# Performance work log

Measured on AMD Instinct MI355X. Metric: run time of the kernel, lower is better.

## Reference

```python
import jax, jax.numpy as jnp
import numpy as np
from jax import lax

B, C, H, W = 16, 3, 64, 64
P = 256        # total_patches
PS = 9         # patch_size
E = 256        # attn_embed_dim
NH = 8         # attn_heads
POSD = 64      # pos_embed_dim
HW = H * W
DH = E // NH


def setup_inputs() -> dict:
    key = jax.random.key(0)
    ks = jax.random.split(key, 20)
    def rn(k, shape, fan_in):
        return jax.random.normal(k, shape, jnp.float32) * (1.0 / np.sqrt(fan_in))
    return {
        "x": jax.random.normal(ks[0], (B, C, H, W), jnp.float32),
        "conv_w": rn(ks[1], (P, C, PS, PS), C * PS * PS),
        "conv_b": jnp.zeros((P,), jnp.float32),
        "in_w": rn(ks[2], (HW, E), HW),
        "in_b": jnp.zeros((E,), jnp.float32),
        "wq": rn(ks[3], (E, E), E), "bq": jnp.zeros((E,), jnp.float32),
        "wk": rn(ks[4], (E, E), E), "bk": jnp.zeros((E,), jnp.float32),
        "wv": rn(ks[5], (E, E), E), "bv": jnp.zeros((E,), jnp.float32),
        "wo": rn(ks[6], (E, E), E), "bo": jnp.zeros((E,), jnp.float32),
        "out_w": rn(ks[7], (E, HW), E),
        "out_b": jnp.zeros((HW,), jnp.float32),
        "fc_w": rn(ks[8], (HW, 2), HW),
        "fc_b": jnp.zeros((2,), jnp.float32),
        "pos_w": rn(ks[9], (2, POSD), 2),
        "pos_b": jnp.zeros((POSD,), jnp.float32),
    }


# pixel-center normalized coords matching affine_grid(align_corners=False)
_BASE = (2.0 * jnp.arange(PS, dtype=jnp.float32) + 1.0) / PS - 1.0


def _sample_patch(img, tx, ty):
    # img: (C,H,W); tx, ty scalars. Replicates affine_grid + grid_sample
    # (bilinear, padding_mode='border', align_corners=False) WITHOUT the
    # full-image repeat of the original module.
    gx = (PS / W) * _BASE[None, :] + tx     # (PS,PS) x-coords
    gy = (PS / H) * _BASE[:, None] + ty     # (PS,PS) y-coords
    ix = ((gx + 1.0) * W - 1.0) * 0.5       # unnormalize, align_corners=False
    iy = ((gy + 1.0) * H - 1.0) * 0.5
    x0 = jnp.floor(ix); y0 = jnp.floor(iy)
    wx = ix - x0;       wy = iy - y0
    x0i = jnp.clip(x0.astype(jnp.int32), 0, W - 1)
    x1i = jnp.clip(x0.astype(jnp.int32) + 1, 0, W - 1)
    y0i = jnp.clip(y0.astype(jnp.int32), 0, H - 1)
    y1i = jnp.clip(y0.astype(jnp.int32) + 1, 0, H - 1)
    v00 = img[:, y0i, x0i]; v01 = img[:, y0i, x1i]
    v10 = img[:, y1i, x0i]; v11 = img[:, y1i, x1i]
    return (v00 * (1 - wx) * (1 - wy) + v01 * wx * (1 - wy)
            + v10 * (1 - wx) * wy + v11 * wx * wy)   # (C,PS,PS)


def _forward(x, conv_w, conv_b, in_w, in_b, wq, bq, wk, bk, wv, bv, wo, bo,
             out_w, out_b, fc_w, fc_b, pos_w, pos_b):
    # ConvBlock: conv (same padding for odd kernel) + ReLU
    feat = lax.conv_general_dilated(
        x, conv_w, (1, 1), [(PS // 2, PS // 2)] * 2,
        dimension_numbers=("NCHW", "OIHW", "NCHW"))
    feat = jax.nn.relu(feat + conv_b[None, :, None, None])   # (B,P,H,W)
    # ConvSelfAttn: tokens are the P channels, features are flattened HxW
    tok = feat.reshape(B, P, HW) @ in_w + in_b                # (B,P,E)
    q = (tok @ wq + bq).reshape(B, P, NH, DH)
    k = (tok @ wk + bk).reshape(B, P, NH, DH)
    v = (tok @ wv + bv).reshape(B, P, NH, DH)
    scores = jnp.einsum("bqhd,bkhd->bhqk", q, k) / np.sqrt(DH)
    attn = jax.nn.softmax(scores, axis=-1)
    o = jnp.einsum("bhqk,bkhd->bqhd", attn, v).reshape(B, P, E)
    o = o @ wo + bo
    feat2 = o @ out_w + out_b                                 # (B,P,HW)
    # translation params in [-1,1]
    tp = jnp.tanh(feat2 @ fc_w + fc_b)                        # (B,P,2)
    tx, ty = tp[..., 0], tp[..., 1]
    sample_bp = jax.vmap(jax.vmap(_sample_patch, in_axes=(None, 0, 0)),
                         in_axes=(0, 0, 0))
    patches = sample_bp(x, tx, ty)                            # (B,P,C,PS,PS)
    patches = patches.reshape(B, P, C * PS * PS)
    pos_embeds = tp @ pos_w + pos_b                           # (B,P,POSD)
    return patches, pos_embeds


def reference(x, conv_w, conv_b, in_w, in_b, wq, bq, wk, bk, wv, bv, wo, bo,
              out_w, out_b, fc_w, fc_b, pos_w, pos_b):
    return _forward(x, conv_w, conv_b, in_w, in_b, wq, bq, wk, bk, wv, bv,
                    wo, bo, out_w, out_b, fc_w, fc_b, pos_w, pos_b)
```

## Files before the change

kernel.cpp:

```cpp
#include <hip/hip_runtime.h>
#include <hip/hip_bf16.h>

#define Bd 16
#define Cd 3
#define Hd 64
#define Wd 64
#define Pd 256
#define PSd 9
#define Ed 256
#define NHd 8
#define DHd 32
#define HWd 4096
#define POSDd 64

typedef unsigned short u16;
typedef short short8 __attribute__((ext_vector_type(8)));
typedef float f32x4 __attribute__((ext_vector_type(4)));

__device__ __forceinline__ float bf2f(u16 u) {
    union { unsigned int i; float f; } c; c.i = ((unsigned int)u) << 16; return c.f;
}
__device__ __forceinline__ u16 f2bf(float f) {
    unsigned int x = __float_as_uint(f);
    unsigned int r = (x + 0x7fffu + ((x >> 16) & 1u)) >> 16;
    return (u16)r;
}

__global__ __launch_bounds__(256) void prep_fused(
    const float* __restrict__ conv_w, const float* __restrict__ in_w,
    const float* __restrict__ wq, const float* __restrict__ wk,
    const float* __restrict__ wv, const float* __restrict__ bq,
    const float* __restrict__ bk, const float* __restrict__ bv,
    const float* __restrict__ out_w, const float* __restrict__ fc_w,
    const float* __restrict__ out_b, const float* __restrict__ fc_b,
    u16* __restrict__ convw_h, u16* __restrict__ convw_l,
    u16* __restrict__ inw_h, u16* __restrict__ inw_l,
    u16* __restrict__ wqkv_h, u16* __restrict__ wqkv_l,
    float* __restrict__ bqkv, float* __restrict__ G, float* __restrict__ h0) {
    __shared__ u16 th[64][65];
    __shared__ u16 tl[64][65];
    int blk = blockIdx.x, t = threadIdx.x;

    if (blk < 256) {
        float v = (t < 243) ? conv_w[blk * 243 + t] : 0.f;
        u16 h = f2bf(v);
        convw_h[blk * 256 + t] = h;
        convw_l[blk * 256 + t] = f2bf(v - bf2f(h));
    } else if (blk < 560) {
        const float* W;
        u16 *Th, *Tl;
        int K, local;
        if (blk < 272)      { W = wq;   Th = wqkv_h;              Tl = wqkv_l;              K = 256;  local = blk - 256; }
        else if (blk < 288) { W = wk;   Th = wqkv_h + 256 * 256;  Tl = wqkv_l + 256 * 256;  K = 256;  local = blk - 272; }
        else if (blk < 304) { W = wv;   Th = wqkv_h + 512 * 256;  Tl = wqkv_l + 512 * 256;  K = 256;  local = blk - 288; }
        else                { W = in_w; Th = inw_h;               Tl = inw_l;               K = 4096; local = blk - 304; }
        int kt = (K == 256) ? (local & 3) : (local & 63);
        int nt = (K == 256) ? (local >> 2) : (local >> 6);
        int k0 = kt * 64, n0 = nt * 64;
        int col = t & 63, r4 = t >> 6;
        #pragma unroll
        for (int i = 0; i < 16; i++) {
            int kr = 4 * i + r4;
            float v = W[(size_t)(k0 + kr) * 256 + n0 + col];
            u16 h = f2bf(v);
            th[col][kr] = h;
            tl[col][kr] = f2bf(v - bf2f(h));
        }
        __syncthreads();
        #pragma unroll
        for (int i = 0; i < 16; i++) {
            int nr = 4 * i + r4;
            Th[(size_t)(n0 + nr) * K + k0 + col] = th[nr][col];
            Tl[(size_t)(n0 + nr) * K + k0 + col] = tl[nr][col];
        }
    } else if (blk == 560) {
        bqkv[t] = bq[t]; bqkv[256 + t] = bk[t]; bqkv[512 + t] = bv[t];
    } else if (blk < 625) {
        int e = (blk - 561) * 4 + (t >> 6);
        int lane = t & 63;
        float a0 = 0.f, a1 = 0.f;
        for (int i = lane; i < HWd; i += 64) {
            float a = out_w[(size_t)e * HWd + i];
            a0 += a * fc_w[2 * i];
            a1 += a * fc_w[2 * i + 1];
        }
        #pragma unroll
        for (int off = 32; off; off >>= 1) { a0 += __shfl_xor(a0, off); a1 += __shfl_xor(a1, off); }
        if (lane == 0) { G[2 * e] = a0; G[2 * e + 1] = a1; }
    } else {
        int wj = t >> 6, lane = t & 63;
        if (wj < 2) {
            float a = 0.f;
            for (int i = lane; i < HWd; i += 64) a += out_b[i] * fc_w[2 * i + wj];
            #pragma unroll
            for (int off = 32; off; off >>= 1) a += __shfl_xor(a, off);
            if (lane == 0) h0[wj] = a + fc_b[wj];
        }
    }
}

__global__ __launch_bounds__(64) void precompute_M2(
    const float* __restrict__ wo, const float* __restrict__ bo,
    const float* __restrict__ G, float* __restrict__ M2, float* __restrict__ h0) {
    int blk = blockIdx.x, lane = threadIdx.x;
    if (blk < 256) {
        float m0 = 0.f, m1 = 0.f;
        for (int f = lane; f < Ed; f += 64) {
            float wv = wo[blk * Ed + f];
            m0 += wv * G[2 * f];
            m1 += wv * G[2 * f + 1];
        }
        #pragma unroll
        for (int off = 32; off; off >>= 1) { m0 += __shfl_xor(m0, off); m1 += __shfl_xor(m1, off); }
        if (lane == 0) { M2[2 * blk] = m0; M2[2 * blk + 1] = m1; }
    } else {
        int j = blk - 256;
        float hh = 0.f;
        for (int f = lane; f < Ed; f += 64) hh += bo[f] * G[2 * f + j];
        #pragma unroll
        for (int off = 32; off; off >>= 1) hh += __shfl_xor(hh, off);
        if (lane == 0) h0[j] += hh;
    }
}

__global__ __launch_bounds__(256, 3) void conv_gemm(
    const u16* __restrict__ Ah, const u16* __restrict__ Al,
    const float* __restrict__ x, const float* __restrict__ conv_b,
    u16* __restrict__ feat_hi, u16* __restrict__ feat_lo) {
    __shared__ u16 sBh[64 * 72], sBl[64 * 72];
    __shared__ float wls[3 * 9 * 72];
    int tid = threadIdx.x;
    int w = tid >> 6, L = tid & 63;
    int m16 = L & 15, qd = L >> 4;
    int y = blockIdx.x;
    int nb = y << 6;
    int b = blockIdx.y;

    for (int i = tid; i < 3 * 9 * 72; i += 256) wls[i] = 0.f;
    __syncthreads();
    for (int i = tid; i < 3 * 9 * 64; i += 256) {
        int c = i / 576, rem = i - c * 576, wr = rem >> 6, col = rem & 63;
        int iy = y - 4 + wr;
        if (iy >= 0 && iy < 64)
            wls[c * 648 + wr * 72 + 4 + col] = x[((b * 3 + c) << 12) + (iy << 6) + col];
    }
    __syncthreads();

    f32x4 acc[4][4];
    #pragma unroll
    for (int mt = 0; mt < 4; mt++)
        #pragma unroll
        for (int ct = 0; ct < 4; ct++) acc[mt][ct] = (f32x4){0.f, 0.f, 0.f, 0.f};

    int n = tid >> 2, kb = (tid & 3) << 4;
    int arow = w * 16 + m16;

    u16 hbuf[16] __attribute__((aligned(8)));
    u16 lbuf[16] __attribute__((aligned(8)));
    auto build = [&](int kbase) {
        #pragma unroll
        for (int j = 0; j < 16; j++) {
            int k = kbase + kb + j;
            float v = 0.f;
            if (k < 243) {
                int c = (k >= 81) + (k >= 162);
                int rem = k - c * 81;
                int dy = (rem * 57) >> 9;
                int dx = rem - dy * 9;
                v = wls[c * 648 + dy * 72 + dx + n];
            }
            u16 h = f2bf(v);
            hbuf[j] = h;
            lbuf[j] = f2bf(v - bf2f(h));
        }
    };
    build(0);

    for (int k0 = 0; k0 < 256; k0 += 64) {
        short8 afh[4][2], afl[4][2];
        #pragma unroll
        for (int mt = 0; mt < 4; mt++)
            #pragma unroll
            for (int c = 0; c < 2; c++) {
                int ao = (mt * 64 + arow) * 256 + k0 + c * 32 + qd * 8;
                afh[mt][c] = *(const short8*)(Ah + ao);
                afl[mt][c] = *(const short8*)(Al + ao);
            }
        __syncthreads();
        #pragma unroll
        for (int t = 0; t < 4; t++) {
            *(ushort4*)&sBh[n * 72 + kb + 4 * t] = *(ushort4*)&hbuf[4 * t];
            *(ushort4*)&sBl[n * 72 + kb + 4 * t] = *(ushort4*)&lbuf[4 * t];
        }
        __syncthreads();
        if (k0 < 192) build(k0 + 64);
        #pragma unroll
        for (int c = 0; c < 2; c++) {
            #pragma unroll
            for (int ct = 0; ct < 4; ct++) {
                int bb = (ct * 16 + m16) * 72 + c * 32 + qd * 8;
                short8 bH = *(const short8*)&sBh[bb];
                short8 bL = *(const short8*)&sBl[bb];
                #pragma unroll
                for (int mt = 0; mt < 4; mt++) {
                    acc[mt][ct] = __builtin_amdgcn_mfma_f32_16x16x32_bf16(afh[mt][c], bH, acc[mt][ct], 0, 0, 0);
                    acc[mt][ct] = __builtin_amdgcn_mfma_f32_16x16x32_bf16(afh[mt][c], bL, acc[mt][ct], 0, 0, 0);
                    acc[mt][ct] = __builtin_amdgcn_mfma_f32_16x16x32_bf16(afl[mt][c], bH, acc[mt][ct], 0, 0, 0);
                }
            }
        }
    }

    #pragma unroll
    for (int mt = 0; mt < 4; mt++) {
        #pragma unroll
        for (int i = 0; i < 4; i++) {
            int gr = mt * 64 + w * 16 + qd * 4 + i;
            float bv = conv_b[gr];
            #pragma unroll
            for (int ct = 0; ct < 4; ct++) {
                int gc = nb + ct * 16 + m16;
                float val = fmaxf(acc[mt][ct][i] + bv, 0.f);
                size_t oi = ((size_t)(b * 256 + gr)) * HWd + gc;
                u16 h = f2bf(val);
                feat_hi[oi] = h;
                feat_lo[oi] = f2bf(val - bf2f(h));
            }
        }
    }
}

__global__ __launch_bounds__(256, 4) void gemm_mfma3(
    const u16* __restrict__ Ah, const u16* __restrict__ Al,
    const u16* __restrict__ Bh, const u16* __restrict__ Bl,
    const float* __restrict__ bias,
    float* __restrict__ Co, u16* __restrict__ Ch, u16* __restrict__ Cl,
    int N, int K, int klen, long long pstride, int mode) {
    __shared__ u16 sAh[64 * 72], sAl[64 * 72], sBh[64 * 72], sBl[64 * 72];
    int tid = threadIdx.x;
    int w = tid >> 6;
    int L = tid & 63;
    int m16 = L & 15, qd = L >> 4;
    int mb = blockIdx.y * 64, nb = blockIdx.x * 64;
    int kbeg = blockIdx.z * klen;

    f32x4 acc[4];
    #pragma unroll
    for (int i = 0; i < 4; i++) acc[i] = (f32x4){0.f, 0.f, 0.f, 0.f};

    int r = tid >> 2, s = tid & 3;
    const u16* pAh = Ah + (size_t)(mb + r) * K + kbeg + s * 16;
    const u16* pAl = Al + (size_t)(mb + r) * K + kbeg + s * 16;
    const u16* pBh = Bh + (size_t)(nb + r) * K + kbeg + s * 16;
    const u16* pBl = Bl + (size_t)(nb + r) * K + kbeg + s * 16;
    u16* dAh = &sAh[r * 72 + s * 16];
    u16* dAl = &sAl[r * 72 + s * 16];
    u16* dBh = &sBh[r * 72 + s * 16];
    u16* dBl = &sBl[r * 72 + s * 16];

    uint4 a0 = *(const uint4*)(pAh);
    uint4 a1 = *(const uint4*)(pAh + 8);
    uint4 a2 = *(const uint4*)(pAl);
    uint4 a3 = *(const uint4*)(pAl + 8);
    uint4 b0 = *(const uint4*)(pBh);
    uint4 b1 = *(const uint4*)(pBh + 8);
    uint4 b2 = *(const uint4*)(pBl);
    uint4 b3 = *(const uint4*)(pBl + 8);

    for (int k0 = 0; k0 < klen; k0 += 64) {
        __syncthreads();
        *(uint4*)(dAh) = a0; *(uint4*)(dAh + 8) = a1;
        *(uint4*)(dAl) = a2; *(uint4*)(dAl + 8) = a3;
        *(uint4*)(dBh) = b0; *(uint4*)(dBh + 8) = b1;
        *(uint4*)(dBl) = b2; *(uint4*)(dBl + 8) = b3;
        __syncthreads();
        int kn = k0 + 64;
        if (kn < klen) {
            a0 = *(const uint4*)(pAh + kn);
            a1 = *(const uint4*)(pAh + kn + 8);
            a2 = *(const uint4*)(pAl + kn);
            a3 = *(const uint4*)(pAl + kn + 8);
            b0 = *(const uint4*)(pBh + kn);
            b1 = *(const uint4*)(pBh + kn + 8);
            b2 = *(const uint4*)(pBl + kn);
            b3 = *(const uint4*)(pBl + kn + 8);
        }
        #pragma unroll
        for (int c = 0; c < 2; c++) {
            int ab = (w * 16 + m16) * 72 + c * 32 + qd * 8;
            short8 aH = *(const short8*)&sAh[ab];
            short8 aL = *(const short8*)&sAl[ab];
            #pragma unroll
            for (int ct = 0; ct < 4; ct++) {
                int bb = (ct * 16 + m16) * 72 + c * 32 + qd * 8;
                short8 bH = *(const short8*)&sBh[bb];
                short8 bL = *(const short8*)&sBl[bb];
                acc[ct] = __builtin_amdgcn_mfma_f32_16x16x32_bf16(aH, bH, acc[ct], 0, 0, 0);
                acc[ct] = __builtin_amdgcn_mfma_f32_16x16x32_bf16(aH, bL, acc[ct], 0, 0, 0);
                acc[ct] = __builtin_amdgcn_mfma_f32_16x16x32_bf16(aL, bH, acc[ct], 0, 0, 0);
            }
        }
    }

    #pragma unroll
    for (int ct = 0; ct < 4; ct++) {
        int gc = nb + ct * 16 + m16;
        float bv = (mode == 2) ? 0.f : bias[gc];
        #pragma unroll
        for (int i = 0; i < 4; i++) {
            int gr = mb + w * 16 + qd * 4 + i;
            float val = acc[ct][i] + bv;
            size_t oi = (size_t)gr * N + gc;
            if (mode == 0) {
                Co[oi] = val;
            } else if (mode == 2) {
                Co[(size_t)blockIdx.z * pstride + oi] = val;
            } else {
                u16 h = f2bf(val);
                Ch[oi] = h;
                Cl[oi] = f2bf(val - bf2f(h));
            }
        }
    }
}

__global__ __launch_bounds__(256) void reduce_split(
    const float* __restrict__ part, const float* __restrict__ bias,
    u16* __restrict__ Ch, u16* __restrict__ Cl, int total) {
    int i = (blockIdx.x * 256 + threadIdx.x) * 4;
    if (i >= total) return;
    float4 s0 = *(const float4*)(part + i);
    float4 s1 = *(const float4*)(part + (size_t)total + i);
    float4 s2 = *(const float4*)(part + 2 * (size_t)total + i);
    float4 s3 = *(const float4*)(part + 3 * (size_t)total + i);
    float4 bv = *(const float4*)(bias + (i & 255));
    float v[4] = { s0.x + s1.x + s2.x + s3.x + bv.x,
                   s0.y + s1.y + s2.y + s3.y + bv.y,
                   s0.z + s1.z + s2.z + s3.z + bv.z,
                   s0.w + s1.w + s2.w + s3.w + bv.w };
    u16 hb[4] __attribute__((aligned(8)));
    u16 lb[4] __attribute__((aligned(8)));
    #pragma unroll
    for (int j = 0; j < 4; j++) {
        u16 h = f2bf(v[j]);
        hb[j] = h;
        lb[j] = f2bf(v[j] - bf2f(h));
    }
    *(ushort4*)(Ch + i) = *(ushort4*)hb;
    *(ushort4*)(Cl + i) = *(ushort4*)lb;
}

__global__ __launch_bounds__(256) void transpose_v(
    const u16* __restrict__ qkvh, const u16* __restrict__ qkvl,
    u16* __restrict__ vTh, u16* __restrict__ vTl) {
    __shared__ u16 th[32][264];
    __shared__ u16 tl[32][264];
    int b = blockIdx.x, h = blockIdx.y;
    int t = threadIdx.x;
    {
        const u16* srch = qkvh + ((size_t)(b * 256 + t)) * 768 + 512 + h * 32;
        const u16* srcl = qkvl + ((size_t)(b * 256 + t)) * 768 + 512 + h * 32;
        #pragma unroll
        for (int j = 0; j < 4; j++) {
            short8 vh = *(const short8*)(srch + j * 8);
            short8 vl = *(const short8*)(srcl + j * 8);
            #pragma unroll
            for (int e = 0; e < 8; e++) {
                th[j * 8 + e][t] = (u16)vh[e];
                tl[j * 8 + e][t] = (u16)vl[e];
            }
        }
    }
    __syncthreads();
    {
        int d = t >> 3, seg = t & 7;
        size_t dst = ((size_t)((b * 8 + h) * 32 + d)) * 256 + seg * 32;
        #pragma unroll
        for (int j = 0; j < 4; j++) {
            *(uint4*)(vTh + dst + j * 8) = *(uint4*)&th[d][seg * 32 + j * 8];
            *(uint4*)(vTl + dst + j * 8) = *(uint4*)&tl[d][seg * 32 + j * 8];
        }
    }
}

__global__ __launch_bounds__(256) void attention_mfma(
    const u16* __restrict__ qkvh, const u16* __restrict__ qkvl,
    const u16* __restrict__ vTh, const u16* __restrict__ vTl,
    float* __restrict__ o) {
    __shared__ u16 ph[4][16][264];
    int b = blockIdx.x, h = blockIdx.y, qc = blockIdx.z;
    int tid = threadIdx.x;
    int w = tid >> 6, L = tid & 63;
    int m16 = L & 15, qd = L >> 4;
    const float rs = 0.17677669529663687f;

    size_t qoff = ((size_t)(b * 256 + qc * 64 + w * 16 + m16)) * 768 + h * 32 + qd * 8;
    short8 qH = *(const short8*)(qkvh + qoff);
    short8 qL = *(const short8*)(qkvl + qoff);

    f32x4 sacc[16];
    #pragma unroll
    for (int nt = 0; nt < 16; nt++) {
        size_t koff = ((size_t)(b * 256 + nt * 16 + m16)) * 768 + 256 + h * 32 + qd * 8;
        short8 bH = *(const short8*)(qkvh + koff);
        short8 bL = *(const short8*)(qkvl + koff);
        f32x4 a = (f32x4){0.f, 0.f, 0.f, 0.f};
        a = __builtin_amdgcn_mfma_f32_16x16x32_bf16(qH, bH, a, 0, 0, 0);
        a = __builtin_amdgcn_mfma_f32_16x16x32_bf16(qH, bL, a, 0, 0, 0);
        a = __builtin_amdgcn_mfma_f32_16x16x32_bf16(qL, bH, a, 0, 0, 0);
        sacc[nt] = a;
    }

    float l4[4] = {0.f, 0.f, 0.f, 0.f};
    #pragma unroll
    for (int nt = 0; nt < 16; nt++)
        #pragma unroll
        for (int i = 0; i < 4; i++) {
            float p = __expf(sacc[nt][i] * rs);
            sacc[nt][i] = p;
            l4[i] += p;
        }
    #pragma unroll
    for (int i = 0; i < 4; i++) {
        l4[i] += __shfl_xor(l4[i], 1);
        l4[i] += __shfl_xor(l4[i], 2);
        l4[i] += __shfl_xor(l4[i], 4);
        l4[i] += __shfl_xor(l4[i], 8);
    }

    #pragma unroll
    for (int nt = 0; nt < 16; nt++)
        #pragma unroll
        for (int i = 0; i < 4; i++)
            ph[w][qd * 4 + i][nt * 16 + m16] = f2bf(sacc[nt][i]);

    f32x4 oacc[2];
    oacc[0] = (f32x4){0.f, 0.f, 0.f, 0.f};
    oacc[1] = (f32x4){0.f, 0.f, 0.f, 0.f};
    size_t vbase = ((size_t)(b * 8 + h)) * 32 * 256;
    #pragma unroll
    for (int kt = 0; kt < 8; kt++) {
        short8 pa = *(const short8*)&ph[w][m16][kt * 32 + qd * 8];
        #pragma unroll
        for (int ct = 0; ct < 2; ct++) {
            size_t voff = vbase + (size_t)(ct * 16 + m16) * 256 + kt * 32 + qd * 8;
            short8 vH = *(const short8*)(vTh + voff);
            short8 vL = *(const short8*)(vTl + voff);
            oacc[ct] = __builtin_amdgcn_mfma_f32_16x16x32_bf16(pa, vH, oacc[ct], 0, 0, 0);
            oacc[ct] = __builtin_amdgcn_mfma_f32_16x16x32_bf16(pa, vL, oacc[ct], 0, 0, 0);
        }
    }

    #pragma unroll
    for (int i = 0; i < 4; i++) {
        float rinv = 1.f / l4[i];
        int orow = b * 256 + qc * 64 + w * 16 + qd * 4 + i;
        #pragma unroll
        for (int ct = 0; ct < 2; ct++)
            o[(size_t)orow * 256 + h * 32 + ct * 16 + m16] = oacc[ct][i] * rinv;
    }
}

#define PATCH_OUT 995328
__global__ __launch_bounds__(256) void head_kernel(
    const float* __restrict__ o, const float* __restrict__ M2,
    const float* __restrict__ h0, const float* __restrict__ pos_w,
    const float* __restrict__ pos_b, const float* __restrict__ x,
    float* __restrict__ out) {
    int w = threadIdx.x >> 6, lane = threadIdx.x & 63;
    int bp = blockIdx.x * 4 + w;
    int b = bp >> 8;

    const float* orow = o + (size_t)bp * Ed;
    float4 o4 = *(const float4*)(orow + lane * 4);
    int e0 = lane * 4;
    float s0 = o4.x * M2[2 * e0 + 0] + o4.y * M2[2 * e0 + 2] + o4.z * M2[2 * e0 + 4] + o4.w * M2[2 * e0 + 6];
    float s1 = o4.x * M2[2 * e0 + 1] + o4.y * M2[2 * e0 + 3] + o4.z * M2[2 * e0 + 5] + o4.w * M2[2 * e0 + 7];
    #pragma unroll
    for (int off = 32; off; off >>= 1) { s0 += __shfl_xor(s0, off); s1 += __shfl_xor(s1, off); }

    float tx = tanhf(s0 + h0[0]);
    float ty = tanhf(s1 + h0[1]);

    {
        float pv = tx * pos_w[lane] + ty * pos_w[64 + lane] + pos_b[lane];
        out[PATCH_OUT + bp * POSDd + lane] = pv;
    }

    const float* xb = x + b * 3 * HWd;
    #pragma unroll
    for (int s = 0; s < 4; s++) {
        int idx = s * 64 + lane;
        if (idx < 243) {
            int c = idx / 81;
            int rem = idx - c * 81;
            int iy = rem / 9;
            int jx = rem - iy * 9;
            float basex = (2.f * jx + 1.f) / 9.f - 1.f;
            float basey = (2.f * iy + 1.f) / 9.f - 1.f;
            float gx = 0.140625f * basex + tx;
            float gy = 0.140625f * basey + ty;
            float ix  = ((gx + 1.f) * 64.f - 1.f) * 0.5f;
            float iyf = ((gy + 1.f) * 64.f - 1.f) * 0.5f;
            float x0f = floorf(ix), y0f = floorf(iyf);
            float wx = ix - x0f, wy = iyf - y0f;
            int x0i = min(max((int)x0f, 0), 63);
            int x1i = min(max((int)x0f + 1, 0), 63);
            int y0i = min(max((int)y0f, 0), 63);
            int y1i = min(max((int)y0f + 1, 0), 63);
            const float* xc = xb + c * HWd;
            float v00 = xc[y0i * Wd + x0i];
            float v01 = xc[y0i * Wd + x1i];
            float v10 = xc[y1i * Wd + x0i];
            float v11 = xc[y1i * Wd + x1i];
            float val = v00 * (1.f - wx) * (1.f - wy) + v01 * wx * (1.f - wy)
                      + v10 * (1.f - wx) * wy + v11 * wx * wy;
            out[bp * 243 + idx] = val;
        }
    }
}

extern "C" void kernel_launch(void* const* d_in, const int* in_sizes, int n_in,
                              void* d_out, int out_size, void* d_ws, size_t ws_size,
                              hipStream_t stream) {
    (void)in_sizes; (void)n_in; (void)out_size;
    const float* x      = (const float*)d_in[0];
    const float* conv_w = (const float*)d_in[1];
    const float* conv_b = (const float*)d_in[2];
    const float* in_w   = (const float*)d_in[3];
    const float* in_b   = (const float*)d_in[4];
    const float* wq     = (const float*)d_in[5];
    const float* bq     = (const float*)d_in[6];
    const float* wk     = (const float*)d_in[7];
    const float* bk     = (const float*)d_in[8];
    const float* wv     = (const float*)d_in[9];
    const float* bv     = (const float*)d_in[10];
    const float* wo     = (const float*)d_in[11];
    const float* bo     = (const float*)d_in[12];
    const float* out_w  = (const float*)d_in[13];
    const float* out_b  = (const float*)d_in[14];
    const float* fc_w   = (const float*)d_in[15];
    const float* fc_b   = (const float*)d_in[16];
    const float* pos_w  = (const float*)d_in[17];
    const float* pos_b  = (const float*)d_in[18];

    int CB = 16;
    for (;;) {
        size_t u16e = (size_t)(2 * CB + 4) * 1048576 + 2 * 196608 + 2 * 65536
                    + 2 * 3145728 + 2 * 1048576;
        size_t f32e = 768 + 1048576 + 4ull * CB * 65536 + 2048;
        if (u16e * 2 + f32e * 4 <= ws_size || CB == 1) break;
        CB >>= 1;
    }
    int nchunks = 16 / CB;

    char* base = (char*)d_ws;
    u16* feat_hi = (u16*)base;
    u16* feat_lo = feat_hi + (size_t)CB * 1048576;
    u16* tok_hi  = feat_lo + (size_t)CB * 1048576;
    u16* tok_lo  = tok_hi + 1048576;
    u16* inw_h   = tok_lo + 1048576;
    u16* inw_l   = inw_h + 1048576;
    u16* wqkv_h  = inw_l + 1048576;
    u16* wqkv_l  = wqkv_h + 196608;
    u16* convw_h = wqkv_l + 196608;
    u16* convw_l = convw_h + 65536;
    u16* qkvh    = convw_l + 65536;
    u16* qkvl    = qkvh + 3145728;
    u16* vTh     = qkvl + 3145728;
    u16* vTl     = vTh + 1048576;
    float* bqkv  = (float*)(vTl + 1048576);
    float* o     = bqkv + 768;
    float* part  = o + 1048576;
    float* G     = part + 4ull * CB * 65536;
    float* M2    = G + 512;
    float* h0    = M2 + 512;
    float* out   = (float*)d_out;

    hipLaunchKernelGGL(prep_fused, dim3(626), dim3(256), 0, stream,
                       conv_w, in_w, wq, wk, wv, bq, bk, bv,
                       out_w, fc_w, out_b, fc_b,
                       convw_h, convw_l, inw_h, inw_l,
                       wqkv_h, wqkv_l, bqkv, G, h0);
    hipLaunchKernelGGL(precompute_M2, dim3(258), dim3(64), 0, stream,
                       wo, bo, G, M2, h0);

    for (int c = 0; c < nchunks; ++c) {
        hipLaunchKernelGGL(conv_gemm, dim3(64, CB), dim3(256), 0, stream,
                           convw_h, convw_l,
                           x + (size_t)c * CB * 3 * HWd, conv_b,
                           feat_hi, feat_lo);
        hipLaunchKernelGGL(gemm_mfma3, dim3(4, CB * 4, 4), dim3(256), 0, stream,
                           feat_hi, feat_lo, inw_h, inw_l, in_b,
                           part, (u16*)nullptr, (u16*)nullptr,
                           256, 4096, 1024, (long long)CB * 65536, 2);
        hipLaunchKernelGGL(reduce_split, dim3(CB * 65536 / 1024), dim3(256), 0, stream,
                           part, in_b,
                           tok_hi + (size_t)c * CB * 65536,
                           tok_lo + (size_t)c * CB * 65536,
                           CB * 65536);
    }
    hipLaunchKernelGGL(gemm_mfma3, dim3(12, 64, 1), dim3(256), 0, stream,
                       tok_hi, tok_lo, wqkv_h, wqkv_l, bqkv,
                       (float*)nullptr, qkvh, qkvl, 768, 256, 256, 0LL, 1);
    hipLaunchKernelGGL(transpose_v, dim3(16, 8), dim3(256), 0, stream,
                       qkvh, qkvl, vTh, vTl);
    hipLaunchKernelGGL(attention_mfma, dim3(16, 8, 4), dim3(256), 0, stream,
                       qkvh, qkvl, vTh, vTl, o);
    hipLaunchKernelGGL(head_kernel, dim3(1024), dim3(256), 0, stream,
                       o, M2, h0, pos_w, pos_b, x, out);
}
```

Before: 256.9 us.

## Fuse V transpose into QKV GEMM epilogue and swizzle split-K block order

Removes the separate transpose_v kernel. The QKV projection GEMM (new mode 3) now also writes V columns straight into the transposed vTh/vTl layout from its epilogue. The split-K input-projection GEMM switches to a 1D grid with a block-index swizzle that groups the 4 N tiles and 8 M/K tiles so that blocks scheduled together share A/B tiles in cache. This saves one launch and a read/write pass over V, but the transposed stores from the epilogue are scattered and uncoalesced.

```diff
diff --git a/kernel.cpp b/kernel.cpp
--- a/kernel.cpp
+++ b/kernel.cpp
@@ -235,14 +235,25 @@
     const u16* __restrict__ Bh, const u16* __restrict__ Bl,
     const float* __restrict__ bias,
     float* __restrict__ Co, u16* __restrict__ Ch, u16* __restrict__ Cl,
-    int N, int K, int klen, long long pstride, int mode) {
+    u16* __restrict__ vTh, u16* __restrict__ vTl,
+    int N, int K, int klen, long long pstride, int mode, int swz, int nmt) {
     __shared__ u16 sAh[64 * 72], sAl[64 * 72], sBh[64 * 72], sBl[64 * 72];
     int tid = threadIdx.x;
     int w = tid >> 6;
     int L = tid & 63;
     int m16 = L & 15, qd = L >> 4;
-    int mb = blockIdx.y * 64, nb = blockIdx.x * 64;
-    int kbeg = blockIdx.z * klen;
+    int mb, nb, kbeg, zidx;
+    if (swz) {
+        int blk = blockIdx.x;
+        int low = blk & 7, nbi = (blk >> 3) & 3, hi = blk >> 5;
+        int idx = low + 8 * hi;
+        int mbi = idx % nmt;
+        zidx = idx / nmt;
+        nb = nbi * 64; mb = mbi * 64; kbeg = zidx * klen;
+    } else {
+        nb = blockIdx.x * 64; mb = blockIdx.y * 64;
+        zidx = blockIdx.z; kbeg = zidx * klen;
+    }
 
     f32x4 acc[4];
     #pragma unroll
@@ -314,11 +325,19 @@
             if (mode == 0) {
                 Co[oi] = val;
             } else if (mode == 2) {
-                Co[(size_t)blockIdx.z * pstride + oi] = val;
+                Co[(size_t)zidx * pstride + oi] = val;
             } else {
                 u16 h = f2bf(val);
+                u16 l = f2bf(val - bf2f(h));
                 Ch[oi] = h;
-                Cl[oi] = f2bf(val - bf2f(h));
+                Cl[oi] = l;
+                if (mode == 3 && gc >= 512) {
+                    int dg = gc - 512, hh = dg >> 5, d = dg & 31;
+                    int bb2 = gr >> 8, kr = gr & 255;
+                    size_t vi = ((size_t)((bb2 * 8 + hh) * 32 + d)) * 256 + kr;
+                    vTh[vi] = h;
+                    vTl[vi] = l;
+                }
             }
         }
     }
@@ -348,39 +367,6 @@
     }
     *(ushort4*)(Ch + i) = *(ushort4*)hb;
     *(ushort4*)(Cl + i) = *(ushort4*)lb;
-}
-
-__global__ __launch_bounds__(256) void transpose_v(
-    const u16* __restrict__ qkvh, const u16* __restrict__ qkvl,
-    u16* __restrict__ vTh, u16* __restrict__ vTl) {
-    __shared__ u16 th[32][264];
-    __shared__ u16 tl[32][264];
-    int b = blockIdx.x, h = blockIdx.y;
-    int t = threadIdx.x;
-    {
-        const u16* srch = qkvh + ((size_t)(b * 256 + t)) * 768 + 512 + h * 32;
-        const u16* srcl = qkvl + ((size_t)(b * 256 + t)) * 768 + 512 + h * 32;
-        #pragma unroll
-        for (int j = 0; j < 4; j++) {
-            short8 vh = *(const short8*)(srch + j * 8);
-            short8 vl = *(const short8*)(srcl + j * 8);
-            #pragma unroll
-            for (int e = 0; e < 8; e++) {
-                th[j * 8 + e][t] = (u16)vh[e];
-                tl[j * 8 + e][t] = (u16)vl[e];
-            }
-        }
-    }
-    __syncthreads();
-    {
-        int d = t >> 3, seg = t & 7;
-        size_t dst = ((size_t)((b * 8 + h) * 32 + d)) * 256 + seg * 32;
-        #pragma unroll
-        for (int j = 0; j < 4; j++) {
-            *(uint4*)(vTh + dst + j * 8) = *(uint4*)&th[d][seg * 32 + j * 8];
-            *(uint4*)(vTl + dst + j * 8) = *(uint4*)&tl[d][seg * 32 + j * 8];
-        }
-    }
 }
 
 __global__ __launch_bounds__(256) void attention_mfma(
@@ -590,10 +576,11 @@
                            convw_h, convw_l,
                            x + (size_t)c * CB * 3 * HWd, conv_b,
                            feat_hi, feat_lo);
-        hipLaunchKernelGGL(gemm_mfma3, dim3(4, CB * 4, 4), dim3(256), 0, stream,
+        hipLaunchKernelGGL(gemm_mfma3, dim3(64 * CB), dim3(256), 0, stream,
                            feat_hi, feat_lo, inw_h, inw_l, in_b,
                            part, (u16*)nullptr, (u16*)nullptr,
-                           256, 4096, 1024, (long long)CB * 65536, 2);
+                           (u16*)nullptr, (u16*)nullptr,
+                           256, 4096, 1024, (long long)CB * 65536, 2, 1, CB * 4);
         hipLaunchKernelGGL(reduce_split, dim3(CB * 65536 / 1024), dim3(256), 0, stream,
                            part, in_b,
                            tok_hi + (size_t)c * CB * 65536,
@@ -602,9 +589,8 @@
     }
     hipLaunchKernelGGL(gemm_mfma3, dim3(12, 64, 1), dim3(256), 0, stream,
                        tok_hi, tok_lo, wqkv_h, wqkv_l, bqkv,
-                       (float*)nullptr, qkvh, qkvl, 768, 256, 256, 0LL, 1);
-    hipLaunchKernelGGL(transpose_v, dim3(16, 8), dim3(256), 0, stream,
-                       qkvh, qkvl, vTh, vTl);
+                       (float*)nullptr, qkvh, qkvl, vTh, vTl,
+                       768, 256, 256, 0LL, 3, 0, 64);
     hipLaunchKernelGGL(attention_mfma, dim3(16, 8, 4), dim3(256), 0, stream,
                        qkvh, qkvl, vTh, vTl, o);
     hipLaunchKernelGGL(head_kernel, dim3(1024), dim3(256), 0, stream,
```

New measurement: 244.1 us. 1.05x faster.
